# Kernel tuning notes

Hardware: AMD Instinct MI355X
Metric: run time of the kernel (lower is better)

## Reference

```python
import jax, jax.numpy as jnp
import numpy as np

N = 8  # fixed node count per sample (hardcoded in the torch module)


def setup_inputs() -> dict:
    key = jax.random.key(0)
    ks = jax.random.split(key, 13)
    B = 131072

    def w(k, shape, fan_in):
        # torch nn.Linear default init: U(-1/sqrt(fan_in), 1/sqrt(fan_in))
        return jax.random.uniform(k, shape, jnp.float32, -1.0, 1.0) / np.sqrt(fan_in).astype(np.float32)

    return {
        "x": jax.random.normal(ks[0], (B, N), jnp.float32),
        "enc_w1": w(ks[1], (3, 64), 3),   "enc_b1": w(ks[2], (64,), 3),
        "enc_w2": w(ks[3], (64, 2), 64),  "enc_b2": w(ks[4], (2,), 64),
        "gcn1_w": w(ks[5], (2, 32), 2),   "gcn1_b": w(ks[6], (32,), 2),
        "gcn2_w": w(ks[7], (32, 32), 32), "gcn2_b": w(ks[8], (32,), 32),
        "dec_w1": w(ks[9], (32, 64), 32), "dec_b1": w(ks[10], (64,), 32),
        "dec_w2": w(ks[11], (64, 3), 64), "dec_b2": w(ks[12], (3,), 64),
    }


def _gabriel_norm_adj(p):
    """Batched Gabriel graph -> GCN-normalized (A + I) with unit edge weights.

    p: (B, N, 2) latent 2D points.
    Edge (i,j) exists iff no other point k lies strictly inside the circle
    with diameter (p_i, p_j)  (dist(p_k, mid)^2 < r^2, matching torch's '<').
    Gabriel graphs contain the nearest-neighbor graph, so for N>=2 edges always
    exist and the torch fallback branch is unreachable.
    Returns D^{-1/2} (A + I) D^{-1/2} of shape (B, N, N) (GCNConv default:
    add_self_loops=True with weight 1, symmetric normalization).
    """
    mid = (p[:, :, None, :] + p[:, None, :, :]) * 0.5                 # (B,N,N,2)
    r2 = jnp.sum((p[:, :, None, :] - mid) ** 2, axis=-1)              # (B,N,N)
    # d2[b,i,j,k] = ||p[b,k] - mid[b,i,j]||^2  -> (B,N,N,N), the big intermediate
    d2 = jnp.sum((p[:, None, None, :, :] - mid[:, :, :, None, :]) ** 2, axis=-1)
    a = jnp.arange(N)
    k_not_ij = (a[None, None, :] != a[:, None, None]) & (a[None, None, :] != a[None, :, None])  # (N,N,N) [i,j,k]
    blocked = jnp.any((d2 < r2[..., None]) & k_not_ij, axis=-1)       # (B,N,N)
    off_diag = a[:, None] != a[None, :]
    adj = ((~blocked) & off_diag).astype(p.dtype)                     # symmetric Gabriel adjacency
    a_hat = adj + jnp.eye(N, dtype=p.dtype)                           # self-loops, weight 1
    dinv = jax.lax.rsqrt(jnp.sum(a_hat, axis=-1))                     # (B,N)
    return dinv[:, :, None] * a_hat * dinv[:, None, :]


def reference(x, enc_w1, enc_b1, enc_w2, enc_b2,
              gcn1_w, gcn1_b, gcn2_w, gcn2_b,
              dec_w1, dec_b1, dec_w2, dec_b2):
    B = x.shape[0]
    idx = jnp.arange(N, dtype=x.dtype)
    # preprocess: (B, N, 3) rows [0, value, index]
    xp = jnp.stack([jnp.zeros_like(x), x, jnp.broadcast_to(idx, x.shape)], axis=-1)
    latent = jax.nn.relu(xp @ enc_w1 + enc_b1) @ enc_w2 + enc_b2      # (B,N,2)
    # torch builds the graph from detach().cpu().numpy() -> no grad through structure
    norm = jax.lax.stop_gradient(_gabriel_norm_adj(latent))           # (B,N,N)
    h1 = jax.nn.relu(jnp.einsum('bij,bjf->bif', norm, latent @ gcn1_w) + gcn1_b)  # (B,N,32)
    h2 = jnp.einsum('bij,bjf->bif', norm, h1 @ gcn2_w) + gcn2_b                    # (B,N,32)
    pooled = jnp.mean(h2, axis=1)                                     # (B,32)
    node = jnp.broadcast_to(pooled[:, None, :], (B, N, pooled.shape[-1]))
    dec = jax.nn.relu(node @ dec_w1 + dec_b1) @ dec_w2 + dec_b2       # (B,N,3)
    reconstructed = dec[:, :, 1]                                      # (B,N)
    return reconstructed, latent
```

## Files before the change

kernel.cpp:

```cpp
#include <hip/hip_runtime.h>


__global__ __launch_bounds__(256, 2) void gae_kernel(
    const float* __restrict__ x,
    const float* __restrict__ enc_w1,
    const float* __restrict__ enc_b1,
    const float* __restrict__ enc_w2,
    const float* __restrict__ enc_b2,
    const float* __restrict__ gcn1_w,
    const float* __restrict__ gcn1_b,
    const float* __restrict__ gcn2_w,
    const float* __restrict__ gcn2_b,
    const float* __restrict__ dec_w1,
    const float* __restrict__ dec_b1,
    const float* __restrict__ dec_w2,
    const float* __restrict__ dec_b2,
    float* __restrict__ out_rec,
    float* __restrict__ out_lat,
    int B)
{
    const int b = blockIdx.x * blockDim.x + threadIdx.x;
    if (b >= B) return;

    float xv[8];
    {
        const float4* xp = reinterpret_cast<const float4*>(x + (size_t)b * 8);
        float4 a = xp[0], c = xp[1];
        xv[0] = a.x; xv[1] = a.y; xv[2] = a.z; xv[3] = a.w;
        xv[4] = c.x; xv[5] = c.y; xv[6] = c.z; xv[7] = c.w;
    }

    float px[8], py[8];
    #pragma unroll
    for (int i = 0; i < 8; ++i) { px[i] = enc_b2[0]; py[i] = enc_b2[1]; }
    #pragma unroll 2
    for (int h = 0; h < 64; ++h) {
        const float wx = enc_w1[64 + h];
        const float wi = enc_w1[128 + h];
        const float bb = enc_b1[h];
        const float ux = enc_w2[2 * h + 0];
        const float uy = enc_w2[2 * h + 1];
        #pragma unroll
        for (int i = 0; i < 8; ++i) {
            float t = fmaf(xv[i], wx, fmaf((float)i, wi, bb));
            t = fmaxf(t, 0.0f);
            px[i] = fmaf(t, ux, px[i]);
            py[i] = fmaf(t, uy, py[i]);
        }
    }

    {
        float4* lo = reinterpret_cast<float4*>(out_lat + (size_t)b * 16);
        lo[0] = make_float4(px[0], py[0], px[1], py[1]);
        lo[1] = make_float4(px[2], py[2], px[3], py[3]);
        lo[2] = make_float4(px[4], py[4], px[5], py[5]);
        lo[3] = make_float4(px[6], py[6], px[7], py[7]);
    }

    unsigned m[8];
    #pragma unroll
    for (int i = 0; i < 8; ++i) m[i] = 1u << i;
    {
        #pragma clang fp contract(off)
        #pragma unroll
        for (int i = 0; i < 8; ++i) {
            #pragma unroll
            for (int j = i + 1; j < 8; ++j) {
                float mx = (px[i] + px[j]) * 0.5f;
                float my = (py[i] + py[j]) * 0.5f;
                float dxi = px[i] - mx, dyi = py[i] - my;
                float r2i = dxi * dxi + dyi * dyi;
                float dxj = px[j] - mx, dyj = py[j] - my;
                float r2j = dxj * dxj + dyj * dyj;
                bool bi = false, bj = false;
                #pragma unroll
                for (int k = 0; k < 8; ++k) {
                    if (k == i || k == j) continue;
                    float dx = px[k] - mx, dy = py[k] - my;
                    float d2 = dx * dx + dy * dy;
                    bi = bi || (d2 < r2i);
                    bj = bj || (d2 < r2j);
                }
                m[i] |= bi ? 0u : (1u << j);
                m[j] |= bj ? 0u : (1u << i);
            }
        }
    }

    float dinv[8];
    #pragma unroll
    for (int i = 0; i < 8; ++i)
        dinv[i] = __builtin_amdgcn_rsqf((float)__popc(m[i]));

    float qx[8], qy[8];
    #pragma unroll
    for (int j = 0; j < 8; ++j) { qx[j] = dinv[j] * px[j]; qy[j] = dinv[j] * py[j]; }

    float nx[8], ny[8];
    #pragma unroll
    for (int i = 0; i < 8; ++i) {
        float sx = 0.0f, sy = 0.0f;
        #pragma unroll
        for (int j = 0; j < 8; ++j) {
            float co = (float)((m[i] >> j) & 1u);
            sx = fmaf(co, qx[j], sx);
            sy = fmaf(co, qy[j], sy);
        }
        nx[i] = dinv[i] * sx;
        ny[i] = dinv[i] * sy;
    }

    float cj[8];
    #pragma unroll
    for (int j = 0; j < 8; ++j) {
        float s = 0.0f;
        #pragma unroll
        for (int i = 0; i < 8; ++i) {
            float co = (float)((m[i] >> j) & 1u);
            s = fmaf(co, dinv[i], s);
        }
        cj[j] = 0.125f * dinv[j] * s;
    }

    float t[32];
    #pragma unroll
    for (int f = 0; f < 32; ++f) t[f] = 0.0f;
    #pragma unroll
    for (int i = 0; i < 8; ++i) {
        #pragma unroll
        for (int f = 0; f < 32; ++f) {
            float h = fmaf(nx[i], gcn1_w[f], fmaf(ny[i], gcn1_w[32 + f], gcn1_b[f]));
            h = fmaxf(h, 0.0f);
            t[f] = fmaf(cj[i], h, t[f]);
        }
    }

    float pooled[32];
    #pragma unroll
    for (int g = 0; g < 32; ++g) {
        float a = gcn2_b[g];
        #pragma unroll
        for (int f = 0; f < 32; ++f) a = fmaf(t[f], gcn2_w[f * 32 + g], a);
        pooled[g] = a;
    }

    float outv = 0.0f;
    #pragma unroll
    for (int h = 0; h < 64; ++h) {
        float a = dec_b1[h];
        #pragma unroll
        for (int f = 0; f < 32; ++f) a = fmaf(pooled[f], dec_w1[f * 64 + h], a);
        outv = fmaf(fmaxf(a, 0.0f), dec_w2[h * 3 + 1], outv);
    }
    outv += dec_b2[1];

    {
        float4 r4 = make_float4(outv, outv, outv, outv);
        float4* ro = reinterpret_cast<float4*>(out_rec + (size_t)b * 8);
        ro[0] = r4;
        ro[1] = r4;
    }
}

extern "C" void kernel_launch(void* const* d_in, const int* in_sizes, int n_in,
                              void* d_out, int out_size, void* d_ws, size_t ws_size,
                              hipStream_t stream) {
    const float* x       = (const float*)d_in[0];
    const float* enc_w1  = (const float*)d_in[1];
    const float* enc_b1  = (const float*)d_in[2];
    const float* enc_w2  = (const float*)d_in[3];
    const float* enc_b2  = (const float*)d_in[4];
    const float* gcn1_w  = (const float*)d_in[5];
    const float* gcn1_b  = (const float*)d_in[6];
    const float* gcn2_w  = (const float*)d_in[7];
    const float* gcn2_b  = (const float*)d_in[8];
    const float* dec_w1  = (const float*)d_in[9];
    const float* dec_b1  = (const float*)d_in[10];
    const float* dec_w2  = (const float*)d_in[11];
    const float* dec_b2  = (const float*)d_in[12];

    const int B = in_sizes[0] / 8;
    float* out_rec = (float*)d_out;
    float* out_lat = out_rec + (size_t)B * 8;

    const int threads = 256;
    const int blocks  = (B + threads - 1) / threads;
    gae_kernel<<<blocks, threads, 0, stream>>>(
        x, enc_w1, enc_b1, enc_w2, enc_b2,
        gcn1_w, gcn1_b, gcn2_w, gcn2_b,
        dec_w1, dec_b1, dec_w2, dec_b2,
        out_rec, out_lat, B);
}
```

Baseline: 115.5 us.

## Vectorize per-sample MLP and GCN math with packed float2 FMA

Rewrites the per-thread compute with two-wide float vectors so the compiler can emit packed FP32 FMA/mul/add instructions across the encoder, GCN and decoder layers. The Gabriel test now takes a min of the candidate distances instead of two boolean OR chains. The adjacency is stored as a float matrix rather than bitmasks, which removes the bit-extract-and-convert work. The decoder is reordered to accumulate all 64 hidden units as packed pairs, which raises register pressure and risks spills under the 2-waves launch bound.

```diff
diff --git a/kernel.cpp b/kernel.cpp
--- a/kernel.cpp
+++ b/kernel.cpp
@@ -1,5 +1,15 @@
 #include <hip/hip_runtime.h>
 
+
+typedef float v2 __attribute__((ext_vector_type(2)));
+
+static __device__ __forceinline__ v2 sp(float s) { return (v2){s, s}; }
+static __device__ __forceinline__ v2 fma2(v2 a, v2 b, v2 c) {
+    return __builtin_elementwise_fma(a, b, c);
+}
+static __device__ __forceinline__ v2 ldv2(const float* p) {
+    return *reinterpret_cast<const v2*>(p);
+}
 
 __global__ __launch_bounds__(256, 2) void gae_kernel(
     const float* __restrict__ x,
@@ -29,130 +39,145 @@
         xv[0] = a.x; xv[1] = a.y; xv[2] = a.z; xv[3] = a.w;
         xv[4] = c.x; xv[5] = c.y; xv[6] = c.z; xv[7] = c.w;
     }
-
-    float px[8], py[8];
-    #pragma unroll
-    for (int i = 0; i < 8; ++i) { px[i] = enc_b2[0]; py[i] = enc_b2[1]; }
-    #pragma unroll 2
+    v2 xv2[4];
+    #pragma unroll
+    for (int ip = 0; ip < 4; ++ip) xv2[ip] = (v2){xv[2 * ip], xv[2 * ip + 1]};
+
+    v2 p[8];
+    {
+        const v2 b2v = ldv2(enc_b2);
+        #pragma unroll
+        for (int i = 0; i < 8; ++i) p[i] = b2v;
+    }
+    #pragma unroll 4
     for (int h = 0; h < 64; ++h) {
         const float wx = enc_w1[64 + h];
         const float wi = enc_w1[128 + h];
         const float bb = enc_b1[h];
-        const float ux = enc_w2[2 * h + 0];
-        const float uy = enc_w2[2 * h + 1];
-        #pragma unroll
-        for (int i = 0; i < 8; ++i) {
-            float t = fmaf(xv[i], wx, fmaf((float)i, wi, bb));
-            t = fmaxf(t, 0.0f);
-            px[i] = fmaf(t, ux, px[i]);
-            py[i] = fmaf(t, uy, py[i]);
+        const v2 uxy = ldv2(enc_w2 + 2 * h);
+        #pragma unroll
+        for (int ip = 0; ip < 4; ++ip) {
+            v2 c2 = fma2((v2){(float)(2 * ip), (float)(2 * ip + 1)}, sp(wi), sp(bb));
+            v2 t2 = fma2(xv2[ip], sp(wx), c2);
+            float t0 = fmaxf(t2.x, 0.0f);
+            float t1 = fmaxf(t2.y, 0.0f);
+            p[2 * ip]     = fma2(sp(t0), uxy, p[2 * ip]);
+            p[2 * ip + 1] = fma2(sp(t1), uxy, p[2 * ip + 1]);
         }
     }
 
     {
         float4* lo = reinterpret_cast<float4*>(out_lat + (size_t)b * 16);
-        lo[0] = make_float4(px[0], py[0], px[1], py[1]);
-        lo[1] = make_float4(px[2], py[2], px[3], py[3]);
-        lo[2] = make_float4(px[4], py[4], px[5], py[5]);
-        lo[3] = make_float4(px[6], py[6], px[7], py[7]);
-    }
-
-    unsigned m[8];
-    #pragma unroll
-    for (int i = 0; i < 8; ++i) m[i] = 1u << i;
+        lo[0] = make_float4(p[0].x, p[0].y, p[1].x, p[1].y);
+        lo[1] = make_float4(p[2].x, p[2].y, p[3].x, p[3].y);
+        lo[2] = make_float4(p[4].x, p[4].y, p[5].x, p[5].y);
+        lo[3] = make_float4(p[6].x, p[6].y, p[7].x, p[7].y);
+    }
+
+    float af[8][8];
+    #pragma unroll
+    for (int i = 0; i < 8; ++i)
+        #pragma unroll
+        for (int j = 0; j < 8; ++j) af[i][j] = (i == j) ? 1.0f : 0.0f;
     {
         #pragma clang fp contract(off)
         #pragma unroll
         for (int i = 0; i < 8; ++i) {
             #pragma unroll
             for (int j = i + 1; j < 8; ++j) {
-                float mx = (px[i] + px[j]) * 0.5f;
-                float my = (py[i] + py[j]) * 0.5f;
-                float dxi = px[i] - mx, dyi = py[i] - my;
-                float r2i = dxi * dxi + dyi * dyi;
-                float dxj = px[j] - mx, dyj = py[j] - my;
-                float r2j = dxj * dxj + dyj * dyj;
-                bool bi = false, bj = false;
+                v2 mid = (p[i] + p[j]) * sp(0.5f);
+                v2 di = p[i] - mid;  v2 si = di * di;  float r2i = si.x + si.y;
+                v2 dj = p[j] - mid;  v2 sj = dj * dj;  float r2j = sj.x + sj.y;
+                float dmin = 3.4e38f;
                 #pragma unroll
                 for (int k = 0; k < 8; ++k) {
                     if (k == i || k == j) continue;
-                    float dx = px[k] - mx, dy = py[k] - my;
-                    float d2 = dx * dx + dy * dy;
-                    bi = bi || (d2 < r2i);
-                    bj = bj || (d2 < r2j);
+                    v2 dk = p[k] - mid;
+                    v2 sk = dk * dk;
+                    dmin = fminf(dmin, sk.x + sk.y);
                 }
-                m[i] |= bi ? 0u : (1u << j);
-                m[j] |= bj ? 0u : (1u << i);
+                af[i][j] = (dmin < r2i) ? 0.0f : 1.0f;
+                af[j][i] = (dmin < r2j) ? 0.0f : 1.0f;
             }
         }
     }
 
     float dinv[8];
     #pragma unroll
-    for (int i = 0; i < 8; ++i)
-        dinv[i] = __builtin_amdgcn_rsqf((float)__popc(m[i]));
-
-    float qx[8], qy[8];
-    #pragma unroll
-    for (int j = 0; j < 8; ++j) { qx[j] = dinv[j] * px[j]; qy[j] = dinv[j] * py[j]; }
-
-    float nx[8], ny[8];
-    #pragma unroll
     for (int i = 0; i < 8; ++i) {
-        float sx = 0.0f, sy = 0.0f;
-        #pragma unroll
-        for (int j = 0; j < 8; ++j) {
-            float co = (float)((m[i] >> j) & 1u);
-            sx = fmaf(co, qx[j], sx);
-            sy = fmaf(co, qy[j], sy);
+        float s = ((af[i][0] + af[i][1]) + (af[i][2] + af[i][3])) +
+                  ((af[i][4] + af[i][5]) + (af[i][6] + af[i][7]));
+        dinv[i] = __builtin_amdgcn_rsqf(s);
+    }
+
+    v2 q[8];
+    #pragma unroll
+    for (int j = 0; j < 8; ++j) q[j] = sp(dinv[j]) * p[j];
+
+    v2 n[8];
+    #pragma unroll
+    for (int i = 0; i < 8; ++i) {
+        v2 acc = sp(af[i][0]) * q[0];
+        #pragma unroll
+        for (int j = 1; j < 8; ++j) acc = fma2(sp(af[i][j]), q[j], acc);
+        n[i] = sp(dinv[i]) * acc;
+    }
+
+    float cj[8];
+    #pragma unroll
+    for (int jp = 0; jp < 4; ++jp) {
+        v2 acc = (v2){af[0][2 * jp], af[0][2 * jp + 1]} * sp(dinv[0]);
+        #pragma unroll
+        for (int i = 1; i < 8; ++i)
+            acc = fma2((v2){af[i][2 * jp], af[i][2 * jp + 1]}, sp(dinv[i]), acc);
+        v2 c2 = (sp(0.125f) * (v2){dinv[2 * jp], dinv[2 * jp + 1]}) * acc;
+        cj[2 * jp] = c2.x; cj[2 * jp + 1] = c2.y;
+    }
+
+    v2 t2[16];
+    #pragma unroll
+    for (int fp = 0; fp < 16; ++fp) t2[fp] = sp(0.0f);
+    #pragma unroll
+    for (int i = 0; i < 8; ++i) {
+        const v2 nxi = sp(n[i].x), nyi = sp(n[i].y), ci = sp(cj[i]);
+        #pragma unroll
+        for (int fp = 0; fp < 16; ++fp) {
+            v2 h = fma2(nxi, ldv2(gcn1_w + 2 * fp),
+                   fma2(nyi, ldv2(gcn1_w + 32 + 2 * fp), ldv2(gcn1_b + 2 * fp)));
+            h = __builtin_elementwise_max(h, sp(0.0f));
+            t2[fp] = fma2(ci, h, t2[fp]);
         }
-        nx[i] = dinv[i] * sx;
-        ny[i] = dinv[i] * sy;
-    }
-
-    float cj[8];
-    #pragma unroll
-    for (int j = 0; j < 8; ++j) {
-        float s = 0.0f;
-        #pragma unroll
-        for (int i = 0; i < 8; ++i) {
-            float co = (float)((m[i] >> j) & 1u);
-            s = fmaf(co, dinv[i], s);
-        }
-        cj[j] = 0.125f * dinv[j] * s;
-    }
-
-    float t[32];
-    #pragma unroll
-    for (int f = 0; f < 32; ++f) t[f] = 0.0f;
-    #pragma unroll
-    for (int i = 0; i < 8; ++i) {
-        #pragma unroll
-        for (int f = 0; f < 32; ++f) {
-            float h = fmaf(nx[i], gcn1_w[f], fmaf(ny[i], gcn1_w[32 + f], gcn1_b[f]));
-            h = fmaxf(h, 0.0f);
-            t[f] = fmaf(cj[i], h, t[f]);
-        }
-    }
-
-    float pooled[32];
-    #pragma unroll
-    for (int g = 0; g < 32; ++g) {
-        float a = gcn2_b[g];
-        #pragma unroll
-        for (int f = 0; f < 32; ++f) a = fmaf(t[f], gcn2_w[f * 32 + g], a);
-        pooled[g] = a;
-    }
-
-    float outv = 0.0f;
-    #pragma unroll
-    for (int h = 0; h < 64; ++h) {
-        float a = dec_b1[h];
-        #pragma unroll
-        for (int f = 0; f < 32; ++f) a = fmaf(pooled[f], dec_w1[f * 64 + h], a);
-        outv = fmaf(fmaxf(a, 0.0f), dec_w2[h * 3 + 1], outv);
-    }
-    outv += dec_b2[1];
+    }
+
+    v2 pooled2[16];
+    #pragma unroll
+    for (int gp = 0; gp < 16; ++gp) pooled2[gp] = ldv2(gcn2_b + 2 * gp);
+    #pragma unroll
+    for (int f = 0; f < 32; ++f) {
+        const v2 tf = sp(t2[f >> 1][f & 1]);
+        #pragma unroll
+        for (int gp = 0; gp < 16; ++gp)
+            pooled2[gp] = fma2(tf, ldv2(gcn2_w + f * 32 + 2 * gp), pooled2[gp]);
+    }
+
+    v2 a2[32];
+    #pragma unroll
+    for (int hp = 0; hp < 32; ++hp) a2[hp] = ldv2(dec_b1 + 2 * hp);
+    #pragma unroll
+    for (int f = 0; f < 32; ++f) {
+        const v2 pf = sp(pooled2[f >> 1][f & 1]);
+        #pragma unroll
+        for (int hp = 0; hp < 32; ++hp)
+            a2[hp] = fma2(pf, ldv2(dec_w1 + f * 64 + 2 * hp), a2[hp]);
+    }
+    float o0 = 0.0f, o1 = 0.0f;
+    #pragma unroll
+    for (int hp = 0; hp < 32; ++hp) {
+        v2 r = __builtin_elementwise_max(a2[hp], sp(0.0f));
+        o0 = fmaf(r.x, dec_w2[(2 * hp) * 3 + 1], o0);
+        o1 = fmaf(r.y, dec_w2[(2 * hp + 1) * 3 + 1], o1);
+    }
+    const float outv = (o0 + o1) + dec_b2[1];
 
     {
         float4 r4 = make_float4(outv, outv, outv, outv);
```

After: 120.5 us. 1.04x slower.
